# Kernel tuning notes

Measured on AMD Instinct MI355X. Metric: run time of the kernel, lower is better.

The kernel has to match this reference:

```python
import jax, jax.numpy as jnp
import numpy as np

F, B, H, N = 2048, 2, 1024, 16
E = H // N  # per-head depth = 64


def setup_inputs() -> dict:
    key = jax.random.key(0)
    k1, k2, k3, k4 = jax.random.split(key, 4)
    q_input = jax.random.normal(k1, (F, B, H), dtype=jnp.float32)
    mask = jax.random.randint(k2, (B, 1, F, F), 0, 2).astype(bool)
    w_qkv = jax.random.normal(k3, (H, 3 * H), dtype=jnp.float32) * 0.02
    b_qkv = jnp.zeros((3 * H,), dtype=jnp.float32)
    w_out = jax.random.normal(k4, (N, E, H), dtype=jnp.float32) * 0.02
    b_out = jnp.zeros((H,), dtype=jnp.float32)
    return {"q_input": q_input, "mask": mask, "w_qkv": w_qkv, "b_qkv": b_qkv,
            "w_out": w_out, "b_out": b_out}


def reference(q_input, mask, w_qkv, b_qkv, w_out, b_out):
    # fused QKV projection: FBH,HD->FBD (+ bias on D)
    qkv = jnp.einsum('fbh,hd->fbd', q_input, w_qkv) + b_qkv          # [F,B,3H]
    qkv = qkv.reshape(F, B, N, 3 * E)
    q, k, v = jnp.split(qkv, 3, axis=-1)                             # each [F,B,N,E]
    scale = 1.0 / jnp.sqrt(jnp.asarray(E, dtype=q.dtype))
    logits = jnp.einsum('fbne,tbne->bnft', q, k) * scale             # [B,N,F,T]
    logits = jnp.where(mask, logits, jnp.asarray(-10000.0, logits.dtype))
    attn_w = jax.nn.softmax(logits, axis=-1)
    ctx = jnp.einsum('bnft,tbne->bnfe', attn_w, v)                   # [B,N,F,E]
    ctx = jnp.transpose(ctx, (2, 0, 1, 3))                           # [F,B,N,E]
    out = jnp.einsum('fbne,ned->fbd', ctx, w_out)                    # [F,B,H] (no bias added)
    return out, b_out
```

## Files before the change

kernel.cpp:

```cpp
#include <hip/hip_runtime.h>
#include <hip/hip_bf16.h>
#include <math.h>

#define F_DIM 2048
#define B_DIM 2
#define H_DIM 1024
#define N_HEADS 16
#define E_DIM 64
#define D3 3072
#define M_DIM 4096

typedef __hip_bfloat16 bf16;
typedef __attribute__((ext_vector_type(8))) __bf16 bf16x8;
typedef __attribute__((ext_vector_type(8))) unsigned short u16x8;
typedef __attribute__((ext_vector_type(4))) float f32x4;

static __device__ __forceinline__ unsigned short f2bf(float f) {
    unsigned u = __float_as_uint(f);
    return (unsigned short)((u + 0x7FFFu + ((u >> 16) & 1u)) >> 16);
}

static __device__ __forceinline__ void glds16(const unsigned short* g, unsigned short* l) {
    __builtin_amdgcn_global_load_lds((const __attribute__((address_space(1))) unsigned int*)g,
                                     (__attribute__((address_space(3))) unsigned int*)l,
                                     16, 0, 0);
}

__global__ void detect_mask_kernel(const int* __restrict__ mask_words, int* __restrict__ flag) {
    __shared__ int red[256];
    int v = mask_words[threadIdx.x];
    red[threadIdx.x] = v & ~1;
    __syncthreads();
    for (int s = 128; s > 0; s >>= 1) {
        if (threadIdx.x < s) red[threadIdx.x] |= red[threadIdx.x + s];
        __syncthreads();
    }
    if (threadIdx.x == 0) *flag = (red[0] != 0) ? 1 : 0;
}

__global__ void pack_mask_kernel(const int* __restrict__ mi, const unsigned char* __restrict__ mu,
                                 const int* __restrict__ flag, unsigned* __restrict__ bits) {
    int w = blockIdx.x * 256 + threadIdx.x;
    size_t base = (size_t)w * 32;
    unsigned out = 0;
    if (*flag) {
        #pragma unroll
        for (int j = 0; j < 32; ++j) out |= (mu[base + j] ? 1u : 0u) << j;
    } else {
        #pragma unroll
        for (int j = 0; j < 32; ++j) out |= (mi[base + j] ? 1u : 0u) << j;
    }
    bits[w] = out;
}

__global__ __launch_bounds__(256) void convert_kernel(const float* __restrict__ in,
                                                      unsigned short* __restrict__ out) {
    int i = (blockIdx.x * 256 + threadIdx.x) * 8;
    float4 a = *(const float4*)&in[i];
    float4 b = *(const float4*)&in[i + 4];
    u16x8 o;
    o[0] = f2bf(a.x); o[1] = f2bf(a.y); o[2] = f2bf(a.z); o[3] = f2bf(a.w);
    o[4] = f2bf(b.x); o[5] = f2bf(b.y); o[6] = f2bf(b.z); o[7] = f2bf(b.w);
    *(u16x8*)&out[i] = o;
}

__global__ __launch_bounds__(256) void transpose_bf16_kernel(const float* __restrict__ in,
                                                             unsigned short* __restrict__ out,
                                                             int R, int C) {
    __shared__ float t[32][33];
    const int c0 = blockIdx.x * 32, r0 = blockIdx.y * 32;
    const int lc = threadIdx.x & 31, lr = threadIdx.x >> 5;
    #pragma unroll
    for (int i = 0; i < 4; ++i) {
        int r = lr + i * 8;
        t[r][lc] = in[(size_t)(r0 + r) * C + c0 + lc];
    }
    __syncthreads();
    #pragma unroll
    for (int i = 0; i < 4; ++i) {
        int r = lr + i * 8;
        out[(size_t)(c0 + r) * R + r0 + lc] = f2bf(t[lc][r]);
    }
}

template<int BM, int BN, bool ADD_BIAS, bool OUT_BF16>
__global__ __launch_bounds__(256) void gemm_bt_kernel(const unsigned short* __restrict__ A,
                                                      const unsigned short* __restrict__ Bt,
                                                      const float* __restrict__ bias,
                                                      void* __restrict__ Cout, int Nc) {
    __shared__ unsigned short Ald[BM * 32];
    __shared__ unsigned short Bld[BN * 32];
    constexpr int WM = BM / 2, WN = BN / 2;
    constexpr int MI = WM / 16, NI = WN / 16;
    constexpr int ACH = BM * 4;
    constexpr int TCH = (BM + BN) * 4;
    const int tid = threadIdx.x;
    const int wave = tid >> 6;
    const int lane = tid & 63;
    const int quad = lane >> 4;
    const int l16 = lane & 15;
    const int wm = (wave & 1) * WM;
    const int wn = (wave >> 1) * WN;
    const int m0 = blockIdx.y * BM;
    const int n0 = blockIdx.x * BN;

    f32x4 acc[MI][NI];
    #pragma unroll
    for (int i = 0; i < MI; ++i)
        #pragma unroll
        for (int j = 0; j < NI; ++j) acc[i][j] = (f32x4){0.f, 0.f, 0.f, 0.f};

    for (int k0 = 0; k0 < 1024; k0 += 32) {
        __syncthreads();
        #pragma unroll
        for (int rr = 0; rr < TCH / 256; ++rr) {
            const int chunk = rr * 256 + tid;
            const int wbase = (rr * 256 + wave * 64) * 8;
            if (chunk < ACH) {
                const int row = chunk >> 2, ko = (chunk & 3) * 8;
                glds16(&A[(size_t)(m0 + row) * 1024 + k0 + ko], &Ald[wbase]);
            } else {
                const int c2 = chunk - ACH;
                const int row = c2 >> 2, ko = (c2 & 3) * 8;
                glds16(&Bt[(size_t)(n0 + row) * 1024 + k0 + ko], &Bld[wbase - ACH * 8]);
            }
        }
        __syncthreads();

        bf16x8 af[MI], bfr[NI];
        #pragma unroll
        for (int i = 0; i < MI; ++i)
            af[i] = *(const bf16x8*)&Ald[(wm + i * 16 + l16) * 32 + quad * 8];
        #pragma unroll
        for (int j = 0; j < NI; ++j)
            bfr[j] = *(const bf16x8*)&Bld[(wn + j * 16 + l16) * 32 + quad * 8];
        #pragma unroll
        for (int mi = 0; mi < MI; ++mi)
            #pragma unroll
            for (int ni = 0; ni < NI; ++ni)
                acc[mi][ni] = __builtin_amdgcn_mfma_f32_16x16x32_bf16(af[mi], bfr[ni], acc[mi][ni], 0, 0, 0);
    }

    #pragma unroll
    for (int ni = 0; ni < NI; ++ni) {
        const int col = n0 + wn + ni * 16 + l16;
        const float bv = ADD_BIAS ? bias[col] : 0.f;
        #pragma unroll
        for (int mi = 0; mi < MI; ++mi) {
            const int rowb = m0 + wm + mi * 16 + quad * 4;
            #pragma unroll
            for (int r = 0; r < 4; ++r) {
                float v = acc[mi][ni][r] + bv;
                if (OUT_BF16) ((unsigned short*)Cout)[(size_t)(rowb + r) * Nc + col] = f2bf(v);
                else          ((float*)Cout)[(size_t)(rowb + r) * Nc + col] = v;
            }
        }
    }
}

#define LSTR 72
__global__ __launch_bounds__(512) void attn_mfma_kernel(const bf16* __restrict__ qkv_,
                                                        const unsigned* __restrict__ mbits,
                                                        unsigned short* __restrict__ ctxb) {
    __shared__ unsigned short K_lds[64 * LSTR];
    __shared__ unsigned short Vt_lds[64 * LSTR];
    __shared__ unsigned short P_lds[128 * LSTR];

    const unsigned short* qkv = (const unsigned short*)qkv_;
    const int tid = threadIdx.x;
    const int wave = tid >> 6;
    const int lane = tid & 63;
    const int quad = lane >> 4;
    const int l16 = lane & 15;
    const int f0 = blockIdx.x * 128;
    const int b = blockIdx.y >> 4;
    const int n = blockIdx.y & 15;
    const int head = n * 192;

    bf16x8 qf[2];
    #pragma unroll
    for (int ks = 0; ks < 2; ++ks) {
        int f = f0 + wave * 16 + l16;
        qf[ks] = *(const bf16x8*)&qkv[(size_t)(f * B_DIM + b) * D3 + head + ks * 32 + quad * 8];
    }

    f32x4 O[4];
    #pragma unroll
    for (int ec = 0; ec < 4; ++ec) O[ec] = (f32x4){0.f, 0.f, 0.f, 0.f};
    float lsum[4] = {0.f, 0.f, 0.f, 0.f};

    unsigned short* Pw = P_lds + wave * 16 * LSTR;
    const float c_exp = 0.18033688011112042f;

    for (int t0 = 0; t0 < F_DIM; t0 += 64) {
        __syncthreads();

        {
            int tr = tid >> 3, e0 = (tid & 7) * 8;
            u16x8 kv = *(const u16x8*)&qkv[(size_t)((t0 + tr) * B_DIM + b) * D3 + head + 64 + e0];
            *(u16x8*)&K_lds[tr * LSTR + e0] = kv;
        }
        if (tid < 256) {
            int tp = tid & 31, e0 = (tid >> 5) * 8;
            u16x8 v0 = *(const u16x8*)&qkv[(size_t)((t0 + 2 * tp) * B_DIM + b) * D3 + head + 128 + e0];
            u16x8 v1 = *(const u16x8*)&qkv[(size_t)((t0 + 2 * tp + 1) * B_DIM + b) * D3 + head + 128 + e0];
            #pragma unroll
            for (int j = 0; j < 8; ++j) {
                unsigned pk = (unsigned)v0[j] | ((unsigned)v1[j] << 16);
                *(unsigned*)&Vt_lds[(e0 + j) * LSTR + 2 * tp] = pk;
            }
        }
        __syncthreads();

        f32x4 S[4];
        #pragma unroll
        for (int ck = 0; ck < 4; ++ck) S[ck] = (f32x4){0.f, 0.f, 0.f, 0.f};
        #pragma unroll
        for (int ck = 0; ck < 4; ++ck) {
            bf16x8 kb0 = *(const bf16x8*)&K_lds[(ck * 16 + l16) * LSTR + quad * 8];
            bf16x8 kb1 = *(const bf16x8*)&K_lds[(ck * 16 + l16) * LSTR + 32 + quad * 8];
            S[ck] = __builtin_amdgcn_mfma_f32_16x16x32_bf16(qf[0], kb0, S[ck], 0, 0, 0);
            S[ck] = __builtin_amdgcn_mfma_f32_16x16x32_bf16(qf[1], kb1, S[ck], 0, 0, 0);
        }

        #pragma unroll
        for (int r = 0; r < 4; ++r) {
            const int row = quad * 4 + r;
            const int f = f0 + wave * 16 + row;
            uint2 wb = *(const uint2*)&mbits[((size_t)b * F_DIM + f) * 64 + (t0 >> 5)];
            #pragma unroll
            for (int ck = 0; ck < 4; ++ck) {
                unsigned wsel = (ck & 2) ? wb.y : wb.x;
                int bit = ((ck & 1) << 4) + l16;
                float p = __builtin_amdgcn_exp2f(S[ck][r] * c_exp);
                p = ((wsel >> bit) & 1u) ? p : 0.f;
                lsum[r] += p;
                Pw[row * LSTR + ck * 16 + l16] = f2bf(p);
            }
        }

        #pragma unroll
        for (int ks = 0; ks < 2; ++ks) {
            bf16x8 pa = *(const bf16x8*)&Pw[l16 * LSTR + ks * 32 + quad * 8];
            #pragma unroll
            for (int ec = 0; ec < 4; ++ec) {
                bf16x8 vb = *(const bf16x8*)&Vt_lds[(ec * 16 + l16) * LSTR + ks * 32 + quad * 8];
                O[ec] = __builtin_amdgcn_mfma_f32_16x16x32_bf16(pa, vb, O[ec], 0, 0, 0);
            }
        }
    }

    #pragma unroll
    for (int r = 0; r < 4; ++r) {
        float l = lsum[r];
        #pragma unroll
        for (int d = 1; d < 16; d <<= 1) l += __shfl_xor(l, d);
        const int f = f0 + wave * 16 + quad * 4 + r;
        const float inv = 1.0f / l;
        #pragma unroll
        for (int ec = 0; ec < 4; ++ec) {
            ctxb[(size_t)(f * B_DIM + b) * H_DIM + n * 64 + ec * 16 + l16] = f2bf(O[ec][r] * inv);
        }
    }
}

__global__ void bout_copy_kernel(const float* __restrict__ b_out, float* __restrict__ dst) {
    int h = blockIdx.x * 256 + threadIdx.x;
    if (h < H_DIM) dst[h] = b_out[h];
}

extern "C" void kernel_launch(void* const* d_in, const int* in_sizes, int n_in,
                              void* d_out, int out_size, void* d_ws, size_t ws_size,
                              hipStream_t stream) {
    const float* q_input = (const float*)d_in[0];
    const void*  mask    = d_in[1];
    const float* w_qkv   = (const float*)d_in[2];
    const float* b_qkv   = (const float*)d_in[3];
    const float* w_out   = (const float*)d_in[4];
    const float* b_out   = (const float*)d_in[5];
    float* out = (float*)d_out;

    char* ws = (char*)d_ws;
    bf16*           qkv     = (bf16*)ws;
    unsigned short* qin_bf  = (unsigned short*)(ws + 25165824);
    unsigned short* ctx     = qin_bf;
    unsigned short* wqkv_bt = (unsigned short*)(ws + 33554432);
    unsigned short* wout_bt = wqkv_bt;
    unsigned*       mbits   = (unsigned*)(ws + 39845888);
    int*            flag    = (int*)(ws + 40894464);

    detect_mask_kernel<<<1, 256, 0, stream>>>((const int*)mask, flag);
    pack_mask_kernel<<<1024, 256, 0, stream>>>((const int*)mask, (const unsigned char*)mask, flag, mbits);

    convert_kernel<<<2048, 256, 0, stream>>>(q_input, qin_bf);
    transpose_bf16_kernel<<<dim3(96, 32), 256, 0, stream>>>(w_qkv, wqkv_bt, 1024, 3072);

    gemm_bt_kernel<128, 128, true, true><<<dim3(24, 32), 256, 0, stream>>>(qin_bf, wqkv_bt, b_qkv, qkv, 3072);

    transpose_bf16_kernel<<<dim3(32, 32), 256, 0, stream>>>(w_out, wout_bt, 1024, 1024);

    attn_mfma_kernel<<<dim3(16, 32), 512, 0, stream>>>(qkv, mbits, ctx);

    gemm_bt_kernel<64, 128, false, false><<<dim3(8, 64), 256, 0, stream>>>(ctx, wout_bt, nullptr, out, 1024);

    bout_copy_kernel<<<4, 256, 0, stream>>>(b_out, out + (size_t)M_DIM * H_DIM);
}
```

Baseline: 248.6 us.

## Fuse prep kernels into one launch and pack P/V LDS writes

Merges mask detection and packing, input conversion, both weight transposes and the bias copy into a single prep kernel. Each block derives the mask-format flag locally with a ballot, which removes the separate detect kernel and several launches. When the workspace is large enough, w_out gets its own buffer so it can be transposed up front; otherwise the old sequence runs. In attention, P is written to LDS as packed 32-bit pairs and the V transpose loads are reordered to match, which changes the column permutation of P and V consistently and cuts LDS store count.

```diff
diff --git a/kernel.cpp b/kernel.cpp
--- a/kernel.cpp
+++ b/kernel.cpp
@@ -24,6 +24,72 @@
     __builtin_amdgcn_global_load_lds((const __attribute__((address_space(1))) unsigned int*)g,
                                      (__attribute__((address_space(3))) unsigned int*)l,
                                      16, 0, 0);
+}
+
+__global__ __launch_bounds__(256) void prep_kernel(const float* __restrict__ q_input,
+                                                   const void* __restrict__ mask,
+                                                   const float* __restrict__ w_qkv,
+                                                   const float* __restrict__ w_out,
+                                                   const float* __restrict__ b_out,
+                                                   unsigned short* __restrict__ qin_bf,
+                                                   unsigned short* __restrict__ wqkv_bt,
+                                                   unsigned short* __restrict__ wout_bt,
+                                                   unsigned* __restrict__ mbits,
+                                                   float* __restrict__ bout_dst) {
+    __shared__ float sh[32 * 33];
+    const int bid = blockIdx.x;
+    const int tid = threadIdx.x;
+
+    if (bid < 2048) {
+        int i = (bid * 256 + tid) * 8;
+        float4 a = *(const float4*)&q_input[i];
+        float4 b = *(const float4*)&q_input[i + 4];
+        u16x8 o;
+        o[0] = f2bf(a.x); o[1] = f2bf(a.y); o[2] = f2bf(a.z); o[3] = f2bf(a.w);
+        o[4] = f2bf(b.x); o[5] = f2bf(b.y); o[6] = f2bf(b.z); o[7] = f2bf(b.w);
+        *(u16x8*)&qin_bf[i] = o;
+    } else if (bid < 6144) {
+        const float* in; unsigned short* out; int R, C, bx, by;
+        if (bid < 5120) { int idx = bid - 2048; in = w_qkv; out = wqkv_bt; R = 1024; C = 3072; bx = idx % 96; by = idx / 96; }
+        else            { int idx = bid - 5120; in = w_out; out = wout_bt; R = 1024; C = 1024; bx = idx % 32; by = idx / 32; }
+        float (*t)[33] = (float(*)[33])sh;
+        const int c0 = bx * 32, r0 = by * 32;
+        const int lc = tid & 31, lr = tid >> 5;
+        #pragma unroll
+        for (int i = 0; i < 4; ++i) {
+            int r = lr + i * 8;
+            t[r][lc] = in[(size_t)(r0 + r) * C + c0 + lc];
+        }
+        __syncthreads();
+        #pragma unroll
+        for (int i = 0; i < 4; ++i) {
+            int r = lr + i * 8;
+            out[(size_t)(c0 + r) * R + r0 + lc] = f2bf(t[lc][r]);
+        }
+    } else if (bid < 7168) {
+        int* shi = (int*)sh;
+        int v = ((const int*)mask)[tid] & ~1;
+        unsigned long long bal = __ballot(v != 0);
+        if ((tid & 63) == 0) shi[tid >> 6] = (bal != 0) ? 1 : 0;
+        __syncthreads();
+        const int byte_mode = shi[0] | shi[1] | shi[2] | shi[3];
+        int w = (bid - 6144) * 256 + tid;
+        size_t base = (size_t)w * 32;
+        unsigned out = 0;
+        if (byte_mode) {
+            const unsigned char* mu = (const unsigned char*)mask;
+            #pragma unroll
+            for (int j = 0; j < 32; ++j) out |= (mu[base + j] ? 1u : 0u) << j;
+        } else {
+            const int* mi = (const int*)mask;
+            #pragma unroll
+            for (int j = 0; j < 32; ++j) out |= (mi[base + j] ? 1u : 0u) << j;
+        }
+        mbits[w] = out;
+    } else {
+        int h = (bid - 7168) * 256 + tid;
+        if (h < H_DIM) bout_dst[h] = b_out[h];
+    }
 }
 
 __global__ void detect_mask_kernel(const int* __restrict__ mask_words, int* __restrict__ flag) {
@@ -81,6 +147,11 @@
         int r = lr + i * 8;
         out[(size_t)(c0 + r) * R + r0 + lc] = f2bf(t[lc][r]);
     }
+}
+
+__global__ void bout_copy_kernel(const float* __restrict__ b_out, float* __restrict__ dst) {
+    int h = blockIdx.x * 256 + threadIdx.x;
+    if (h < H_DIM) dst[h] = b_out[h];
 }
 
 template<int BM, int BN, bool ADD_BIAS, bool OUT_BF16>
@@ -201,13 +272,14 @@
             *(u16x8*)&K_lds[tr * LSTR + e0] = kv;
         }
         if (tid < 256) {
-            int tp = tid & 31, e0 = (tid >> 5) * 8;
-            u16x8 v0 = *(const u16x8*)&qkv[(size_t)((t0 + 2 * tp) * B_DIM + b) * D3 + head + 128 + e0];
-            u16x8 v1 = *(const u16x8*)&qkv[(size_t)((t0 + 2 * tp + 1) * B_DIM + b) * D3 + head + 128 + e0];
+            int u = tid & 15, h = (tid >> 4) & 1, e0 = (tid >> 5) * 8;
+            int ta = t0 + h * 32 + u;
+            u16x8 v0 = *(const u16x8*)&qkv[(size_t)(ta * B_DIM + b) * D3 + head + 128 + e0];
+            u16x8 v1 = *(const u16x8*)&qkv[(size_t)((ta + 16) * B_DIM + b) * D3 + head + 128 + e0];
             #pragma unroll
             for (int j = 0; j < 8; ++j) {
                 unsigned pk = (unsigned)v0[j] | ((unsigned)v1[j] << 16);
-                *(unsigned*)&Vt_lds[(e0 + j) * LSTR + 2 * tp] = pk;
+                *(unsigned*)&Vt_lds[(e0 + j) * LSTR + h * 32 + 2 * u] = pk;
             }
         }
         __syncthreads();
@@ -228,15 +300,19 @@
             const int row = quad * 4 + r;
             const int f = f0 + wave * 16 + row;
             uint2 wb = *(const uint2*)&mbits[((size_t)b * F_DIM + f) * 64 + (t0 >> 5)];
+            float p[4];
             #pragma unroll
             for (int ck = 0; ck < 4; ++ck) {
                 unsigned wsel = (ck & 2) ? wb.y : wb.x;
                 int bit = ((ck & 1) << 4) + l16;
-                float p = __builtin_amdgcn_exp2f(S[ck][r] * c_exp);
-                p = ((wsel >> bit) & 1u) ? p : 0.f;
-                lsum[r] += p;
-                Pw[row * LSTR + ck * 16 + l16] = f2bf(p);
-            }
+                float pv = __builtin_amdgcn_exp2f(S[ck][r] * c_exp);
+                p[ck] = ((wsel >> bit) & 1u) ? pv : 0.f;
+            }
+            lsum[r] += (p[0] + p[1]) + (p[2] + p[3]);
+            unsigned pk01 = (unsigned)f2bf(p[0]) | ((unsigned)f2bf(p[1]) << 16);
+            unsigned pk23 = (unsigned)f2bf(p[2]) | ((unsigned)f2bf(p[3]) << 16);
+            *(unsigned*)&Pw[row * LSTR + 2 * l16] = pk01;
+            *(unsigned*)&Pw[row * LSTR + 32 + 2 * l16] = pk23;
         }
 
         #pragma unroll
@@ -262,11 +338,6 @@
             ctxb[(size_t)(f * B_DIM + b) * H_DIM + n * 64 + ec * 16 + l16] = f2bf(O[ec][r] * inv);
         }
     }
-}
-
-__global__ void bout_copy_kernel(const float* __restrict__ b_out, float* __restrict__ dst) {
-    int h = blockIdx.x * 256 + threadIdx.x;
-    if (h < H_DIM) dst[h] = b_out[h];
 }
 
 extern "C" void kernel_launch(void* const* d_in, const int* in_sizes, int n_in,
@@ -279,29 +350,41 @@
     const float* w_out   = (const float*)d_in[4];
     const float* b_out   = (const float*)d_in[5];
     float* out = (float*)d_out;
-
     char* ws = (char*)d_ws;
-    bf16*           qkv     = (bf16*)ws;
-    unsigned short* qin_bf  = (unsigned short*)(ws + 25165824);
-    unsigned short* ctx     = qin_bf;
-    unsigned short* wqkv_bt = (unsigned short*)(ws + 33554432);
-    unsigned short* wout_bt = wqkv_bt;
-    unsigned*       mbits   = (unsigned*)(ws + 39845888);
-    int*            flag    = (int*)(ws + 40894464);
-
-    detect_mask_kernel<<<1, 256, 0, stream>>>((const int*)mask, flag);
-    pack_mask_kernel<<<1024, 256, 0, stream>>>((const int*)mask, (const unsigned char*)mask, flag, mbits);
-
-    convert_kernel<<<2048, 256, 0, stream>>>(q_input, qin_bf);
-    transpose_bf16_kernel<<<dim3(96, 32), 256, 0, stream>>>(w_qkv, wqkv_bt, 1024, 3072);
-
-    gemm_bt_kernel<128, 128, true, true><<<dim3(24, 32), 256, 0, stream>>>(qin_bf, wqkv_bt, b_qkv, qkv, 3072);
-
-    transpose_bf16_kernel<<<dim3(32, 32), 256, 0, stream>>>(w_out, wout_bt, 1024, 1024);
-
-    attn_mfma_kernel<<<dim3(16, 32), 512, 0, stream>>>(qkv, mbits, ctx);
-
-    gemm_bt_kernel<64, 128, false, false><<<dim3(8, 64), 256, 0, stream>>>(ctx, wout_bt, nullptr, out, 1024);
-
-    bout_copy_kernel<<<4, 256, 0, stream>>>(b_out, out + (size_t)M_DIM * H_DIM);
-}
+
+    const size_t FUSED_WS = 25165824ull + 8388608 + 6291456 + 2097152 + 1048576;
+
+    if (ws_size >= FUSED_WS) {
+        bf16*           qkv     = (bf16*)ws;
+        unsigned short* qin_bf  = (unsigned short*)(ws + 25165824);
+        unsigned short* ctx     = qin_bf;
+        unsigned short* wqkv_bt = (unsigned short*)(ws + 33554432);
+        unsigned short* wout_bt = (unsigned short*)(ws + 39845888);
+        unsigned*       mbits   = (unsigned*)(ws + 41943040);
+
+        prep_kernel<<<7172, 256, 0, stream>>>(q_input, mask, w_qkv, w_out, b_out,
+                                              qin_bf, wqkv_bt, wout_bt, mbits,
+                                              out + (size_t)M_DIM * H_DIM);
+        gemm_bt_kernel<128, 128, true, true><<<dim3(24, 32), 256, 0, stream>>>(qin_bf, wqkv_bt, b_qkv, qkv, 3072);
+        attn_mfma_kernel<<<dim3(16, 32), 512, 0, stream>>>(qkv, mbits, ctx);
+        gemm_bt_kernel<64, 128, false, false><<<dim3(8, 64), 256, 0, stream>>>(ctx, wout_bt, nullptr, out, 1024);
+    } else {
+        bf16*           qkv     = (bf16*)ws;
+        unsigned short* qin_bf  = (unsigned short*)(ws + 25165824);
+        unsigned short* ctx     = qin_bf;
+        unsigned short* wqkv_bt = (unsigned short*)(ws + 33554432);
+        unsigned short* wout_bt = wqkv_bt;
+        unsigned*       mbits   = (unsigned*)(ws + 39845888);
+        int*            flag    = (int*)(ws + 40894464);
+
+        detect_mask_kernel<<<1, 256, 0, stream>>>((const int*)mask, flag);
+        pack_mask_kernel<<<1024, 256, 0, stream>>>((const int*)mask, (const unsigned char*)mask, flag, mbits);
+        convert_kernel<<<2048, 256, 0, stream>>>(q_input, qin_bf);
+        transpose_bf16_kernel<<<dim3(96, 32), 256, 0, stream>>>(w_qkv, wqkv_bt, 1024, 3072);
+        gemm_bt_kernel<128, 128, true, true><<<dim3(24, 32), 256, 0, stream>>>(qin_bf, wqkv_bt, b_qkv, qkv, 3072);
+        transpose_bf16_kernel<<<dim3(32, 32), 256, 0, stream>>>(w_out, wout_bt, 1024, 1024);
+        attn_mfma_kernel<<<dim3(16, 32), 512, 0, stream>>>(qkv, mbits, ctx);
+        gemm_bt_kernel<64, 128, false, false><<<dim3(8, 64), 256, 0, stream>>>(ctx, wout_bt, nullptr, out, 1024);
+        bout_copy_kernel<<<4, 256, 0, stream>>>(b_out, out + (size_t)M_DIM * H_DIM);
+    }
+}
```

Result: faster. 239.2 us (-3.8%).
